# Performance work log

Measured on AMD Instinct MI355X. Metric: run time of the kernel, lower is better.

Reference implementation:

```python
import jax, jax.numpy as jnp
import numpy as np
from jax import lax

N_WAY, N_SUPPORT, N_QUERY = 16, 256, 512
D_IN, D_EMB = 4096, 1024
N_CLUSTERS, MAX_ITER = 5, 100


def setup_inputs() -> dict:
    key = jax.random.key(0)
    k1, k2, kw, kb = jax.random.split(key, 4)
    support = jax.random.normal(k1, (N_WAY, N_SUPPORT, D_IN), jnp.float32)
    query = jax.random.normal(k2, (N_WAY, N_QUERY, D_IN), jnp.float32)
    W = jax.random.normal(kw, (D_IN, D_EMB), jnp.float32) / np.float32(np.sqrt(D_IN))
    b = jax.random.normal(kb, (D_EMB,), jnp.float32) * 0.01
    return {"support": support, "query": query, "W": W, "b": b}


def _sqdist(x, c):
    # x [n,d], c [k,d] -> [n,k] squared euclidean distances
    return (jnp.sum(x * x, -1, keepdims=True)
            - 2.0 * (x @ c.T)
            + jnp.sum(c * c, -1))


def _kmeans(x, init):
    # x [n,d], init [k,d]; fixed-iteration Lloyd's kmeans (converged state is a
    # fixed point of the update, matching the torch early-break semantics).
    n = x.shape[0]
    ones = jnp.ones((n,), x.dtype)

    def step(c, _):
        assign = jnp.argmin(_sqdist(x, c), axis=1)              # [n]
        sums = jax.ops.segment_sum(x, assign, num_segments=N_CLUSTERS)
        cnt = jax.ops.segment_sum(ones, assign, num_segments=N_CLUSTERS)
        # empty cluster keeps its old centroid
        new_c = jnp.where(cnt[:, None] > 0,
                          sums / jnp.maximum(cnt, 1.0)[:, None], c)
        return new_c, None

    c, _ = lax.scan(step, init, None, length=MAX_ITER)
    return c


def _forward(support, query, W, b):
    # encoder: shared linear over flattened (n_way * n) rows
    s = (support.reshape(-1, D_IN) @ W + b).reshape(N_WAY, N_SUPPORT, D_EMB)
    q = (query.reshape(-1, D_IN) @ W + b).reshape(N_WAY, N_QUERY, D_EMB)

    # per-class kmeans init: random subset of that class's support embeddings
    keys = jax.random.split(jax.random.key(42), N_WAY)

    def init_fn(key, class_emb):
        idx = jax.random.permutation(key, N_SUPPORT)[:N_CLUSTERS]
        return class_emb[idx]

    inits = jax.vmap(init_fn)(keys, s)                 # [n_way, k, d]
    cluster_protos = jax.vmap(_kmeans)(s, inits)       # [n_way, k, d]
    class_protos = cluster_protos.mean(axis=1)         # [n_way, d]

    # cdist(query_emb [b,n,d], protos [c,d]) -> [b,n,c]
    d2 = (jnp.sum(q * q, -1)[..., None]
          - 2.0 * jnp.einsum('bnd,cd->bnc', q, class_protos)
          + jnp.sum(class_protos * class_protos, -1))
    distances = jnp.sqrt(jnp.maximum(d2, 0.0))
    return -distances                                  # logits [n_way, n_query, n_classes]


def reference(support, query, W, b):
    return _forward(support, query, W, b)
```

## Files before the change

kernel.cpp:

```cpp
#include <hip/hip_runtime.h>
#include <cstdint>
#include <cstddef>


typedef __attribute__((ext_vector_type(4))) float f32x4;
typedef __attribute__((ext_vector_type(8))) short s16x8;
typedef __attribute__((ext_vector_type(4))) short s16x4;
typedef __attribute__((ext_vector_type(8))) __bf16 bf16x8;

__device__ __forceinline__ unsigned short f2bf(float f) {
  unsigned u = __float_as_uint(f);
  return (unsigned short)((u + 0x7FFFu + ((u >> 16) & 1u)) >> 16);
}
__device__ __forceinline__ float bf2f(unsigned short h) {
  return __uint_as_float(((unsigned)h) << 16);
}

typedef const __attribute__((address_space(1))) void GV;
typedef __attribute__((address_space(3))) void LV;
__device__ __forceinline__ void gload_lds16(const void* g, void* l) {
  __builtin_amdgcn_global_load_lds((GV*)g, (LV*)l, 16, 0, 0);
}
__device__ __forceinline__ f32x4 mfma16(bf16x8 a, bf16x8 b, f32x4 c) {
  return __builtin_amdgcn_mfma_f32_16x16x32_bf16(a, b, c, 0, 0, 0);
}
__device__ __forceinline__ float wave_sum(float v) {
#pragma unroll
  for (int st = 1; st < 64; st <<= 1) v += __shfl_xor(v, st);
  return v;
}

__device__ __forceinline__ void tf2x32(unsigned k0, unsigned k1, unsigned x0,
                                       unsigned x1, unsigned& y0, unsigned& y1) {
  unsigned ks0 = k0, ks1 = k1, ks2 = k0 ^ k1 ^ 0x1BD11BDAu;
  x0 += ks0; x1 += ks1;
  const int rA[4] = {13, 15, 26, 6};
  const int rB[4] = {17, 29, 16, 24};
#define ROTL(v, d) (((v) << (d)) | ((v) >> (32 - (d))))
#define RG(R)                                     \
  _Pragma("unroll") for (int i = 0; i < 4; i++) { \
    x0 += x1; x1 = ROTL(x1, R[i]); x1 ^= x0;      \
  }
  RG(rA); x0 += ks1; x1 += ks2 + 1u;
  RG(rB); x0 += ks2; x1 += ks0 + 2u;
  RG(rA); x0 += ks0; x1 += ks1 + 3u;
  RG(rB); x0 += ks1; x1 += ks2 + 4u;
  RG(rA); x0 += ks2; x1 += ks0 + 5u;
#undef RG
#undef ROTL
  y0 = x0; y1 = x1;
}

__global__ __launch_bounds__(256) void prep_sw_k(
    const float* __restrict__ W, const float* __restrict__ sup,
    short* __restrict__ WhiT, short* __restrict__ WloT,
    short* __restrict__ Shi, short* __restrict__ Slo) {
  __shared__ float tile[64][65];
  int t = threadIdx.x;
  if (blockIdx.x < 1024) {
    int bk = blockIdx.x & 63, bn = blockIdx.x >> 6;
#pragma unroll
    for (int i = 0; i < 4; i++) {
      int row = i * 16 + (t >> 4);
      int col = (t & 15) * 4;
      f32x4 v =
          *(const f32x4*)(W + (size_t)(bk * 64 + row) * 1024 + bn * 64 + col);
      tile[row][col + 0] = v[0]; tile[row][col + 1] = v[1];
      tile[row][col + 2] = v[2]; tile[row][col + 3] = v[3];
    }
    __syncthreads();
#pragma unroll
    for (int i = 0; i < 4; i++) {
      int nrow = i * 16 + (t >> 4);
      int kcol = (t & 15) * 4;
      s16x4 hv, lv;
#pragma unroll
      for (int e = 0; e < 4; e++) {
        float v = tile[kcol + e][nrow];
        unsigned short h = f2bf(v);
        hv[e] = (short)h;
        lv[e] = (short)f2bf(v - bf2f(h));
      }
      size_t off = (size_t)(bn * 64 + nrow) * 4096 + bk * 64 + kcol;
      *(s16x4*)(WhiT + off) = hv;
      *(s16x4*)(WloT + off) = lv;
    }
  } else {
    const size_t sup_n8 = (size_t)4096 * 4096 / 8;
    size_t stride = (size_t)(gridDim.x - 1024) * 256;
    for (size_t gid = (size_t)(blockIdx.x - 1024) * 256 + t; gid < sup_n8;
         gid += stride) {
      const float* src = sup + gid * 8;
      f32x4 v0 = *(const f32x4*)src, v1 = *(const f32x4*)(src + 4);
      s16x8 h, l;
#pragma unroll
      for (int e = 0; e < 4; e++) {
        unsigned short hh = f2bf(v0[e]);
        h[e] = (short)hh; l[e] = (short)f2bf(v0[e] - bf2f(hh));
      }
#pragma unroll
      for (int e = 0; e < 4; e++) {
        unsigned short hh = f2bf(v1[e]);
        h[4 + e] = (short)hh; l[4 + e] = (short)f2bf(v1[e] - bf2f(hh));
      }
      *(s16x8*)(Shi + gid * 8) = h;
      *(s16x8*)(Slo + gid * 8) = l;
    }
  }
}

__global__ __launch_bounds__(256) void gemm_supq_k(
    const short* __restrict__ Shi, const short* __restrict__ Slo,
    const short* __restrict__ WhiT, const short* __restrict__ WloT,
    const float* __restrict__ bias, float* __restrict__ emb,
    const float* __restrict__ qry, short* __restrict__ Qhi) {
  __shared__ short lds[24576];
  const int t = threadIdx.x;
  if (blockIdx.x < 512) {
    short* Ah = lds;
    short* Al = lds + 4096;
    short* Bh = lds + 8192;
    short* Bl = lds + 16384;
    const int bid = blockIdx.x;
    const int bm = bid & 63, bn = bid >> 6;
    const int lane = t & 63, w = t >> 6;
    const int wr = w >> 1, wc = w & 1;
    const int fr = lane & 15, kg = lane >> 4;
    const int ls = lane >> 3, lc = lane & 7;
    const short* Ag = Shi + (size_t)bm * 64 * 4096;
    const short* Alg = Slo + (size_t)bm * 64 * 4096;
    f32x4 acc[2][4] = {};

    for (int kt = 0; kt < 64; ++kt) {
      const int k0 = kt * 64;
      __syncthreads();
      const int cch = (lc ^ ls) * 8;
#pragma unroll
      for (int j = 0; j < 2; j++) {
        int rowl = w * 16 + j * 8 + ls;
        size_t aoff = (size_t)rowl * 4096 + k0 + cch;
        int ldst = (w * 16 + j * 8) * 64;
        gload_lds16(Ag + aoff, Ah + ldst);
        gload_lds16(Alg + aoff, Al + ldst);
      }
#pragma unroll
      for (int j = 0; j < 4; j++) {
        int rowl = w * 32 + j * 8 + ls;
        size_t boff = (size_t)(bn * 128 + rowl) * 4096 + k0 + cch;
        int ldst = (w * 32 + j * 8) * 64;
        gload_lds16(WhiT + boff, Bh + ldst);
        gload_lds16(WloT + boff, Bl + ldst);
      }
      __syncthreads();
#pragma unroll
      for (int ks = 0; ks < 2; ++ks) {
        const int cx = ((ks * 4 + kg) ^ (fr & 7)) * 8;
        bf16x8 ahf[2], alf[2], bhf[4], blf[4];
#pragma unroll
        for (int mi = 0; mi < 2; mi++) {
          int arow = wr * 32 + mi * 16 + fr;
          ahf[mi] =
              __builtin_bit_cast(bf16x8, *(const s16x8*)(Ah + arow * 64 + cx));
          alf[mi] =
              __builtin_bit_cast(bf16x8, *(const s16x8*)(Al + arow * 64 + cx));
        }
#pragma unroll
        for (int ni = 0; ni < 4; ni++) {
          int brow = wc * 64 + ni * 16 + fr;
          bhf[ni] =
              __builtin_bit_cast(bf16x8, *(const s16x8*)(Bh + brow * 64 + cx));
          blf[ni] =
              __builtin_bit_cast(bf16x8, *(const s16x8*)(Bl + brow * 64 + cx));
        }
#pragma unroll
        for (int mi = 0; mi < 2; mi++)
#pragma unroll
          for (int ni = 0; ni < 4; ni++) {
            acc[mi][ni] = mfma16(ahf[mi], bhf[ni], acc[mi][ni]);
            acc[mi][ni] = mfma16(ahf[mi], blf[ni], acc[mi][ni]);
            acc[mi][ni] = mfma16(alf[mi], bhf[ni], acc[mi][ni]);
          }
      }
    }
#pragma unroll
    for (int ni = 0; ni < 4; ni++) {
      int gc = bn * 128 + wc * 64 + ni * 16 + fr;
      float bv = bias[gc];
#pragma unroll
      for (int mi = 0; mi < 2; mi++) {
        int gr = bm * 64 + wr * 32 + mi * 16 + kg * 4;
#pragma unroll
        for (int r = 0; r < 4; r++)
          emb[(size_t)(gr + r) * 1024 + gc] = acc[mi][ni][r] + bv;
      }
    }
  } else {
    const size_t qry_n8 = (size_t)8192 * 4096 / 8;
    size_t stride = (size_t)(gridDim.x - 512) * 256;
    for (size_t gid = (size_t)(blockIdx.x - 512) * 256 + t; gid < qry_n8;
         gid += stride) {
      const float* src = qry + gid * 8;
      f32x4 v0 = *(const f32x4*)src, v1 = *(const f32x4*)(src + 4);
      s16x8 h;
#pragma unroll
      for (int e = 0; e < 4; e++) h[e] = (short)f2bf(v0[e]);
#pragma unroll
      for (int e = 0; e < 4; e++) h[4 + e] = (short)f2bf(v1[e]);
      *(s16x8*)(Qhi + gid * 8) = h;
    }
  }
}

__global__ __launch_bounds__(256) void gemm_qry_diag_k(
    const short* __restrict__ Qhi, const short* __restrict__ WhiT,
    const float* __restrict__ bias, float* __restrict__ emb,
    float* __restrict__ G) {
  __shared__ short lds[16384];
  const int t = threadIdx.x;
  if (blockIdx.x < 512) {
    short* Ah = lds;
    short* Bh = lds + 8192;
    const int bid = blockIdx.x;
    const int bm = bid & 63, bn = bid >> 6;
    const int lane = t & 63, w = t >> 6;
    const int wr = w >> 1, wc = w & 1;
    const int fr = lane & 15, kg = lane >> 4;
    const int ls = lane >> 3, lc = lane & 7;
    const short* Ag = Qhi + (size_t)bm * 128 * 4096;
    f32x4 acc[4][4] = {};

    for (int kt = 0; kt < 64; ++kt) {
      const int k0 = kt * 64;
      __syncthreads();
      const int cch = (lc ^ ls) * 8;
#pragma unroll
      for (int j = 0; j < 4; j++) {
        int rowl = w * 32 + j * 8 + ls;
        size_t aoff = (size_t)rowl * 4096 + k0 + cch;
        size_t boff = (size_t)(bn * 128 + rowl) * 4096 + k0 + cch;
        int ldst = (w * 32 + j * 8) * 64;
        gload_lds16(Ag + aoff, Ah + ldst);
        gload_lds16(WhiT + boff, Bh + ldst);
      }
      __syncthreads();
#pragma unroll
      for (int ks = 0; ks < 2; ++ks) {
        const int cx = ((ks * 4 + kg) ^ (fr & 7)) * 8;
        bf16x8 ahf[4], bhf[4];
#pragma unroll
        for (int mi = 0; mi < 4; mi++) {
          int arow = wr * 64 + mi * 16 + fr;
          ahf[mi] =
              __builtin_bit_cast(bf16x8, *(const s16x8*)(Ah + arow * 64 + cx));
        }
#pragma unroll
        for (int ni = 0; ni < 4; ni++) {
          int brow = wc * 64 + ni * 16 + fr;
          bhf[ni] =
              __builtin_bit_cast(bf16x8, *(const s16x8*)(Bh + brow * 64 + cx));
        }
#pragma unroll
        for (int mi = 0; mi < 4; mi++)
#pragma unroll
          for (int ni = 0; ni < 4; ni++)
            acc[mi][ni] = mfma16(ahf[mi], bhf[ni], acc[mi][ni]);
      }
    }
#pragma unroll
    for (int ni = 0; ni < 4; ni++) {
      int gc = bn * 128 + wc * 64 + ni * 16 + fr;
      float bv = bias[gc];
#pragma unroll
      for (int mi = 0; mi < 4; mi++) {
        int gr = 4096 + bm * 128 + wr * 64 + mi * 16 + kg * 4;
#pragma unroll
        for (int r = 0; r < 4; r++)
          emb[(size_t)(gr + r) * 1024 + gc] = acc[mi][ni][r] + bv;
      }
    }
  } else {
    int r = (blockIdx.x - 512) * 4 + (t >> 6);
    int lane = t & 63;
    const float* x = emb + (size_t)r * 1024;
    double acc = 0.0;
#pragma unroll
    for (int ch = 0; ch < 16; ch++) {
      float v = x[ch * 64 + lane];
      acc = fma((double)v, (double)v, acc);
    }
#pragma unroll
    for (int st = 1; st < 64; st <<= 1) acc += __shfl_xor(acc, st);
    if (lane == 0) {
      int c = r >> 8, i = r & 255;
      G[(size_t)c * 65536 + (size_t)i * 256 + i] = (float)acc;
    }
  }
}

__global__ __launch_bounds__(256) void gram_km_k(const float* __restrict__ emb,
                                                 float* __restrict__ G) {
  int c = blockIdx.x >> 4, tl = blockIdx.x & 15, ti = tl >> 2, tj = tl & 3;
  __shared__ float AsT[32][68];
  __shared__ float BsT[32][68];
  int t = threadIdx.x, ty = t >> 4, tx = t & 15;
  const float* base = emb + (size_t)c * 256 * 1024;
  float acc[4][4] = {};
  for (int k0 = 0; k0 < 1024; k0 += 32) {
    __syncthreads();
    {
      int r = t >> 2, seg = t & 3;
      const float* pa = base + (size_t)(ti * 64 + r) * 1024 + k0 + seg * 8;
      f32x4 va0 = *(const f32x4*)pa, va1 = *(const f32x4*)(pa + 4);
#pragma unroll
      for (int e = 0; e < 4; e++) AsT[seg * 8 + e][r] = va0[e];
#pragma unroll
      for (int e = 0; e < 4; e++) AsT[seg * 8 + 4 + e][r] = va1[e];
      const float* pb = base + (size_t)(tj * 64 + r) * 1024 + k0 + seg * 8;
      f32x4 vb0 = *(const f32x4*)pb, vb1 = *(const f32x4*)(pb + 4);
#pragma unroll
      for (int e = 0; e < 4; e++) BsT[seg * 8 + e][r] = vb0[e];
#pragma unroll
      for (int e = 0; e < 4; e++) BsT[seg * 8 + 4 + e][r] = vb1[e];
    }
    __syncthreads();
#pragma unroll 4
    for (int kk = 0; kk < 32; kk++) {
      f32x4 av = *(const f32x4*)(&AsT[kk][ty * 4]);
      f32x4 bv = *(const f32x4*)(&BsT[kk][tx * 4]);
#pragma unroll
      for (int jdx = 0; jdx < 4; jdx++) {
        acc[0][jdx] = fmaf(av[0], bv[jdx], acc[0][jdx]);
        acc[1][jdx] = fmaf(av[1], bv[jdx], acc[1][jdx]);
        acc[2][jdx] = fmaf(av[2], bv[jdx], acc[2][jdx]);
        acc[3][jdx] = fmaf(av[3], bv[jdx], acc[3][jdx]);
      }
    }
  }
#pragma unroll
  for (int i = 0; i < 4; i++) {
    int gr = ti * 64 + ty * 4 + i;
#pragma unroll
    for (int j = 0; j < 4; j++) {
      int gcl = tj * 64 + tx * 4 + j;
      if (gr != gcl)
        G[(size_t)c * 65536 + (size_t)gr * 256 + gcl] = acc[i][j];
    }
  }
}

__global__ __launch_bounds__(256) void gemm_all_k(
    const float* __restrict__ sup, const float* __restrict__ qry,
    const short* __restrict__ WhiT, const short* __restrict__ WloT,
    const float* __restrict__ bias, float* __restrict__ emb) {
  __shared__ short lds[4 * 128 * 64];
  short* Ah = lds;
  short* Al = lds + 8192;
  short* Bh = lds + 16384;
  short* Bl = lds + 24576;
  const int bid = blockIdx.x;
  const int bm = bid % 96, bn = bid / 96;
  const bool is_sup = bm < 32;
  const int t = threadIdx.x, lane = t & 63, w = t >> 6;
  const int wr = w >> 1, wc = w & 1;
  const int fr = lane & 15, kg = lane >> 4;
  const float* Abase = is_sup ? (sup + (size_t)bm * 128 * 4096)
                              : (qry + (size_t)(bm - 32) * 128 * 4096);
  f32x4 acc[4][4] = {};
  const int ls = lane >> 3, lc = lane & 7;

  for (int kt = 0; kt < 64; ++kt) {
    const int k0 = kt * 64;
    __syncthreads();
#pragma unroll
    for (int i = 0; i < 4; i++) {
      int row = i * 32 + w * 8 + ls;
      const float* src = Abase + (size_t)row * 4096 + k0 + lc * 8;
      f32x4 v0 = *(const f32x4*)src;
      f32x4 v1 = *(const f32x4*)(src + 4);
      s16x8 hs;
#pragma unroll
      for (int e = 0; e < 4; e++) hs[e] = (short)f2bf(v0[e]);
#pragma unroll
      for (int e = 0; e < 4; e++) hs[4 + e] = (short)f2bf(v1[e]);
      int chunk = lc ^ (row & 7);
      *(s16x8*)(Ah + row * 64 + chunk * 8) = hs;
      if (is_sup) {
        s16x8 lsv;
#pragma unroll
        for (int e = 0; e < 4; e++)
          lsv[e] = (short)f2bf(v0[e] - bf2f((unsigned short)hs[e]));
#pragma unroll
        for (int e = 0; e < 4; e++)
          lsv[4 + e] = (short)f2bf(v1[e] - bf2f((unsigned short)hs[4 + e]));
        *(s16x8*)(Al + row * 64 + chunk * 8) = lsv;
      }
    }
#pragma unroll
    for (int j = 0; j < 4; j++) {
      int rowl = w * 32 + j * 8 + ls;
      int cch = (lc ^ (ls & 7)) * 8;
      size_t goff = (size_t)(bn * 128 + rowl) * 4096 + k0 + cch;
      gload_lds16(WhiT + goff, Bh + (w * 32 + j * 8) * 64);
      if (is_sup) gload_lds16(WloT + goff, Bl + (w * 32 + j * 8) * 64);
    }
    __syncthreads();
#pragma unroll
    for (int ks = 0; ks < 2; ++ks) {
      const int cx = ((ks * 4 + kg) ^ (fr & 7)) * 8;
      bf16x8 ahf[4], bhf[4];
#pragma unroll
      for (int mi = 0; mi < 4; mi++) {
        int arow = wr * 64 + mi * 16 + fr;
        ahf[mi] = __builtin_bit_cast(bf16x8, *(const s16x8*)(Ah + arow * 64 + cx));
      }
#pragma unroll
      for (int ni = 0; ni < 4; ni++) {
        int brow = wc * 64 + ni * 16 + fr;
        bhf[ni] = __builtin_bit_cast(bf16x8, *(const s16x8*)(Bh + brow * 64 + cx));
      }
      if (is_sup) {
        bf16x8 alf[4], blf[4];
#pragma unroll
        for (int mi = 0; mi < 4; mi++) {
          int arow = wr * 64 + mi * 16 + fr;
          alf[mi] =
              __builtin_bit_cast(bf16x8, *(const s16x8*)(Al + arow * 64 + cx));
        }
#pragma unroll
        for (int ni = 0; ni < 4; ni++) {
          int brow = wc * 64 + ni * 16 + fr;
          blf[ni] =
              __builtin_bit_cast(bf16x8, *(const s16x8*)(Bl + brow * 64 + cx));
        }
#pragma unroll
        for (int mi = 0; mi < 4; mi++)
#pragma unroll
          for (int ni = 0; ni < 4; ni++) {
            acc[mi][ni] = mfma16(ahf[mi], bhf[ni], acc[mi][ni]);
            acc[mi][ni] = mfma16(ahf[mi], blf[ni], acc[mi][ni]);
            acc[mi][ni] = mfma16(alf[mi], bhf[ni], acc[mi][ni]);
          }
      } else {
#pragma unroll
        for (int mi = 0; mi < 4; mi++)
#pragma unroll
          for (int ni = 0; ni < 4; ni++)
            acc[mi][ni] = mfma16(ahf[mi], bhf[ni], acc[mi][ni]);
      }
    }
  }
#pragma unroll
  for (int ni = 0; ni < 4; ni++) {
    int gc = bn * 128 + wc * 64 + ni * 16 + fr;
    float bv = bias[gc];
#pragma unroll
    for (int mi = 0; mi < 4; mi++) {
      int gr = bm * 128 + wr * 64 + mi * 16 + kg * 4;
#pragma unroll
      for (int r = 0; r < 4; r++)
        emb[(size_t)(gr + r) * 1024 + gc] = acc[mi][ni][r] + bv;
    }
  }
}

__global__ __launch_bounds__(256) void diag_k(const float* __restrict__ emb,
                                              float* __restrict__ G) {
  int r = blockIdx.x * 4 + (threadIdx.x >> 6);
  int lane = threadIdx.x & 63;
  const float* x = emb + (size_t)r * 1024;
  double acc = 0.0;
#pragma unroll
  for (int ch = 0; ch < 16; ch++) {
    float v = x[ch * 64 + lane];
    acc = fma((double)v, (double)v, acc);
  }
#pragma unroll
  for (int st = 1; st < 64; st <<= 1) acc += __shfl_xor(acc, st);
  if (lane == 0) {
    int c = r >> 8, i = r & 255;
    G[(size_t)c * 65536 + (size_t)i * 256 + i] = (float)acc;
  }
}

#define APPLY1(db, nb, gg, p)                        \
  if ((db) & 1u)  s[p][0] += ((nb) & 1u)  ? (gg) : -(gg); \
  if ((db) & 2u)  s[p][1] += ((nb) & 2u)  ? (gg) : -(gg); \
  if ((db) & 4u)  s[p][2] += ((nb) & 4u)  ? (gg) : -(gg); \
  if ((db) & 8u)  s[p][3] += ((nb) & 8u)  ? (gg) : -(gg); \
  if ((db) & 16u) s[p][4] += ((nb) & 16u) ? (gg) : -(gg);

__global__ __launch_bounds__(64) void kmeans3_k(const float* __restrict__ G,
                                                float* __restrict__ wts) {
  const int c = blockIdx.x;
  const int lane = threadIdx.x;
  unsigned o0, o1, s0k, s1k;
  tf2x32(0u, 42u, 0u, (unsigned)c, o0, o1);
  tf2x32(o0, o1, 0u, 1u, s0k, s1k);
  unsigned long long key[4];
#pragma unroll
  for (int q = 0; q < 4; q++) {
    unsigned y0, y1;
    tf2x32(s0k, s1k, 0u, (unsigned)(lane + 64 * q), y0, y1);
    key[q] = ((unsigned long long)(y0 ^ y1) << 32) | (unsigned)(lane + 64 * q);
  }
  int idx5[5];
#pragma unroll
  for (int r = 0; r < 5; r++) {
    unsigned long long mn = key[0];
#pragma unroll
    for (int q = 1; q < 4; q++) mn = key[q] < mn ? key[q] : mn;
#pragma unroll
    for (int st = 1; st < 64; st <<= 1) {
      unsigned long long o = __shfl_xor(mn, st);
      mn = o < mn ? o : mn;
    }
    int widx = (int)(unsigned)(mn & 0xffffffffu);
    idx5[r] = widx;
#pragma unroll
    for (int q = 0; q < 4; q++)
      if (widx == lane + 64 * q) key[q] = ~0ull;
  }
  unsigned m[4];
#pragma unroll
  for (int q = 0; q < 4; q++) {
    unsigned mm = 0;
#pragma unroll
    for (int k = 0; k < 5; k++)
      if (idx5[k] == lane + 64 * q) mm |= 1u << k;
    m[q] = mm;
  }
  const float* Gc = G + (size_t)c * 65536;
  float s[4][5];
#pragma unroll
  for (int k = 0; k < 5; k++) {
    const float* row = Gc + (size_t)idx5[k] * 256;
#pragma unroll
    for (int q = 0; q < 4; q++) s[q][k] = row[lane + 64 * q];
  }
  float Minv[5] = {1.0f, 1.0f, 1.0f, 1.0f, 1.0f};

  for (int it = 0; it < 100; ++it) {
    float Tu[5], C2[5];
#pragma unroll
    for (int k = 0; k < 5; k++) {
      float v = 0.0f;
#pragma unroll
      for (int q = 0; q < 4; q++)
        v += ((m[q] >> k) & 1u) ? s[q][k] : 0.0f;
#pragma unroll
      for (int st = 1; st < 64; st <<= 1) v += __shfl_xor(v, st);
      float iv = Minv[k];
      Tu[k] = v * iv * iv;
      C2[k] = -2.0f * iv;
    }
    int a[4];
#pragma unroll
    for (int q = 0; q < 4; q++) {
      float d0 = fmaf(C2[0], s[q][0], Tu[0]);
      float d1 = fmaf(C2[1], s[q][1], Tu[1]);
      float d2 = fmaf(C2[2], s[q][2], Tu[2]);
      float d3 = fmaf(C2[3], s[q][3], Tu[3]);
      float d4 = fmaf(C2[4], s[q][4], Tu[4]);
      int at = 0;
      float dmn = d0;
      if (d1 < dmn) { dmn = d1; at = 1; }
      if (d2 < dmn) { dmn = d2; at = 2; }
      if (d3 < dmn) { dmn = d3; at = 3; }
      if (d4 < dmn) { dmn = d4; at = 4; }
      a[q] = at;
    }
    int cnt[5];
#pragma unroll
    for (int k = 0; k < 5; k++) {
      int v = (a[0] == k) + (a[1] == k) + (a[2] == k) + (a[3] == k);
#pragma unroll
      for (int st = 1; st < 64; st <<= 1) v += __shfl_xor(v, st);
      cnt[k] = v;
    }
    unsigned nm[4], dm[4];
#pragma unroll
    for (int q = 0; q < 4; q++) {
      unsigned nv = 0;
#pragma unroll
      for (int k = 0; k < 5; k++) {
        int bit = (cnt[k] > 0) ? (a[q] == k ? 1 : 0) : (int)((m[q] >> k) & 1u);
        nv |= ((unsigned)bit) << k;
      }
      nm[q] = nv;
      dm[q] = nv ^ m[q];
    }
    unsigned long long bal[4];
#pragma unroll
    for (int q = 0; q < 4; q++) bal[q] = __ballot(dm[q] != 0);
    if ((bal[0] | bal[1] | bal[2] | bal[3]) == 0) break;
#pragma unroll
    for (int q = 0; q < 4; q++) m[q] = nm[q];
#pragma unroll
    for (int k = 0; k < 5; k++)
      if (cnt[k] > 0) Minv[k] = 1.0f / (float)cnt[k];
#pragma unroll
    for (int q = 0; q < 4; q++) {
      unsigned long long mask = bal[q];
      while (mask) {
#define GATHER(i)                                                      \
        int j##i = -1;                                                 \
        unsigned d##i = 0, e##i = 0;                                   \
        float g##i##0 = 0, g##i##1 = 0, g##i##2 = 0, g##i##3 = 0;      \
        if (mask) {                                                    \
          j##i = __builtin_ctzll(mask);                                \
          mask &= mask - 1;                                            \
          d##i = __shfl(dm[q], j##i);                                  \
          e##i = __shfl(nm[q], j##i);                                  \
          const float* row = Gc + (size_t)(q * 64 + j##i) * 256 + lane;\
          g##i##0 = row[0];  g##i##1 = row[64];                        \
          g##i##2 = row[128]; g##i##3 = row[192];                      \
        }
        GATHER(0) GATHER(1) GATHER(2) GATHER(3)
        GATHER(4) GATHER(5) GATHER(6) GATHER(7)
#undef GATHER
#define DOAPPLY(i)                        \
        if (j##i >= 0) {                  \
          APPLY1(d##i, e##i, g##i##0, 0)  \
          APPLY1(d##i, e##i, g##i##1, 1)  \
          APPLY1(d##i, e##i, g##i##2, 2)  \
          APPLY1(d##i, e##i, g##i##3, 3)  \
        }
        DOAPPLY(0) DOAPPLY(1) DOAPPLY(2) DOAPPLY(3)
        DOAPPLY(4) DOAPPLY(5) DOAPPLY(6) DOAPPLY(7)
#undef DOAPPLY
      }
    }
  }
#pragma unroll
  for (int q = 0; q < 4; q++) {
    float wv = 0.0f;
#pragma unroll
    for (int k = 0; k < 5; k++)
      if ((m[q] >> k) & 1u) wv += 0.2f * Minv[k];
    wts[c * 256 + lane + 64 * q] = wv;
  }
}

__global__ __launch_bounds__(256) void proto1_k(const float* __restrict__ emb,
                                                const float* __restrict__ wts,
                                                float* __restrict__ part) {
  int c = blockIdx.x & 15, seg = blockIdx.x >> 4, t = threadIdx.x;
  __shared__ float wl[16];
  if (t < 16) wl[t] = wts[c * 256 + seg * 16 + t];
  __syncthreads();
  f32x4 acc = {};
  const float* base = emb + (size_t)(c * 256 + seg * 16) * 1024 + t * 4;
#pragma unroll
  for (int j = 0; j < 16; j++) {
    f32x4 v = *(const f32x4*)(base + (size_t)j * 1024);
    float wj = wl[j];
#pragma unroll
    for (int e = 0; e < 4; e++) acc[e] = fmaf(wj, v[e], acc[e]);
  }
  *(f32x4*)(part + ((size_t)seg * 16 + c) * 1024 + t * 4) = acc;
}

__global__ __launch_bounds__(256) void proto2_k(const float* __restrict__ part,
                                                float* __restrict__ protos) {
  int c = blockIdx.x, t = threadIdx.x;
  f32x4 acc = {};
#pragma unroll
  for (int seg = 0; seg < 16; seg++) {
    f32x4 v = *(const f32x4*)(part + ((size_t)seg * 16 + c) * 1024 + t * 4);
#pragma unroll
    for (int e = 0; e < 4; e++) acc[e] += v[e];
  }
  *(f32x4*)(protos + (size_t)c * 1024 + t * 4) = acc;
}

__global__ __launch_bounds__(256) void proto_k(const float* __restrict__ emb,
                                               const float* __restrict__ wts,
                                               float* __restrict__ protos) {
  int c = blockIdx.x, t = threadIdx.x;
  __shared__ float wl[256];
  wl[t] = wts[c * 256 + t];
  __syncthreads();
  f32x4 acc = {};
  const float* base = emb + (size_t)c * 256 * 1024 + t * 4;
  for (int j = 0; j < 256; j++) {
    f32x4 v = *(const f32x4*)(base + (size_t)j * 1024);
    float wj = wl[j];
#pragma unroll
    for (int e = 0; e < 4; e++) acc[e] = fmaf(wj, v[e], acc[e]);
  }
  *(f32x4*)(protos + (size_t)c * 1024 + t * 4) = acc;
}

__global__ __launch_bounds__(256) void dist_k(const float* __restrict__ emb,
                                              const float* __restrict__ protos,
                                              float* __restrict__ out) {
  __shared__ float P[16 * 1024];
  int t = threadIdx.x, lane = t & 63, w = t >> 6;
#pragma unroll
  for (int i = 0; i < 16; i++) {
    int off = i * 1024 + t * 4;
    *(f32x4*)(P + off) = *(const f32x4*)(protos + off);
  }
  __syncthreads();
  float psq_keep = 0.0f;
  for (int p = 0; p < 16; p++) {
    float partial = 0.0f;
#pragma unroll
    for (int ch = 0; ch < 16; ch++) {
      float x = P[p * 1024 + ch * 64 + lane];
      partial = fmaf(x, x, partial);
    }
    partial = wave_sum(partial);
    if (lane == p) psq_keep = partial;
  }
  const float* qbase = emb + (size_t)4096 * 1024;
  int r0 = blockIdx.x * 16 + w * 4;
  for (int ri = 0; ri < 4; ri++) {
    int row = r0 + ri;
    const float* q = qbase + (size_t)row * 1024;
    float qv[16];
#pragma unroll
    for (int ch = 0; ch < 16; ch++) qv[ch] = q[ch * 64 + lane];
    float qsq = 0.0f;
#pragma unroll
    for (int ch = 0; ch < 16; ch++) qsq = fmaf(qv[ch], qv[ch], qsq);
    qsq = wave_sum(qsq);
    float dsel = 0.0f;
    for (int p = 0; p < 16; p++) {
      float dp = 0.0f;
#pragma unroll
      for (int ch = 0; ch < 16; ch++)
        dp = fmaf(qv[ch], P[p * 1024 + ch * 64 + lane], dp);
      dp = wave_sum(dp);
      if (lane == p) dsel = dp;
    }
    if (lane < 16) {
      float d2 = qsq - 2.0f * dsel + psq_keep;
      d2 = fmaxf(d2, 0.0f);
      out[(size_t)row * 16 + lane] = -sqrtf(d2);
    }
  }
}

extern "C" void kernel_launch(void* const* d_in, const int* in_sizes, int n_in,
                              void* d_out, int out_size, void* d_ws,
                              size_t ws_size, hipStream_t stream) {
  const float* sup = (const float*)d_in[0];
  const float* qry = (const float*)d_in[1];
  const float* W = (const float*)d_in[2];
  const float* b = (const float*)d_in[3];
  float* out = (float*)d_out;
  char* ws = (char*)d_ws;
  (void)in_sizes; (void)n_in; (void)out_size;

  const size_t NEED_FAST = 206651392ULL;
  if (ws_size >= NEED_FAST) {
    short* WhiT = (short*)(ws + 0);
    short* WloT = (short*)(ws + 8388608);
    short* Shi = (short*)(ws + 16777216);
    short* Slo = (short*)(ws + 50331648);
    short* Qhi = (short*)(ws + 83886080);
    float* emb = (float*)(ws + 150994944);
    float* G = (float*)(ws + 201326592);
    float* wts = (float*)(ws + 205520896);
    float* protos = (float*)(ws + 205537280);
    float* part = (float*)(ws + 205602816);

    prep_sw_k<<<2048, 256, 0, stream>>>(W, sup, WhiT, WloT, Shi, Slo);
    gemm_supq_k<<<768, 256, 0, stream>>>(Shi, Slo, WhiT, WloT, b, emb, qry,
                                         Qhi);
    gemm_qry_diag_k<<<1536, 256, 0, stream>>>(Qhi, WhiT, b, emb, G);
    gram_km_k<<<256, 256, 0, stream>>>(emb, G);
    kmeans3_k<<<16, 64, 0, stream>>>(G, wts);
    proto1_k<<<256, 256, 0, stream>>>(emb, wts, part);
    proto2_k<<<16, 256, 0, stream>>>(part, protos);
    dist_k<<<512, 256, 0, stream>>>(emb, protos, out);
  } else {
    short* WhiT = (short*)(ws + 0);
    short* WloT = (short*)(ws + 8388608);
    float* emb = (float*)(ws + 16777216);
    float* G = (float*)(ws + 67108864);
    float* wts = (float*)(ws + 71303168);
    float* protos = (float*)(ws + 71319552);

    prep_sw_k<<<1024, 256, 0, stream>>>(W, sup, WhiT, WloT, (short*)0,
                                        (short*)0);
    gemm_all_k<<<768, 256, 0, stream>>>(sup, qry, WhiT, WloT, b, emb);
    gram_km_k<<<256, 256, 0, stream>>>(emb, G);
    diag_k<<<1024, 256, 0, stream>>>(emb, G);
    kmeans3_k<<<16, 64, 0, stream>>>(G, wts);
    proto_k<<<16, 256, 0, stream>>>(emb, wts, protos);
    dist_k<<<512, 256, 0, stream>>>(emb, protos, out);
  }
}
```

Before: 446.3 us.

## Fuse query GEMM with distance computation and merge gram with diagonal kernel

The query-embedding GEMM is moved after the kmeans stage and now computes partial query-prototype dot products and squared norms straight from the accumulator tile, so the query embeddings are never written to global memory. A small reduction kernel combines the per-column-block partials with precomputed prototype norms to form the logits. The gram and diagonal kernels are merged into one launch. In exchange, the query GEMM no longer overlaps with the gram computation, the fused kernel uses more shared memory, and the distance is assembled from fp32 partial sums in a different order.

```diff
diff --git a/kernel.cpp b/kernel.cpp
--- a/kernel.cpp
+++ b/kernel.cpp
@@ -211,76 +211,59 @@
   }
 }
 
-__global__ __launch_bounds__(256) void gemm_qry_diag_k(
-    const short* __restrict__ Qhi, const short* __restrict__ WhiT,
-    const float* __restrict__ bias, float* __restrict__ emb,
-    float* __restrict__ G) {
-  __shared__ short lds[16384];
-  const int t = threadIdx.x;
-  if (blockIdx.x < 512) {
-    short* Ah = lds;
-    short* Bh = lds + 8192;
-    const int bid = blockIdx.x;
-    const int bm = bid & 63, bn = bid >> 6;
-    const int lane = t & 63, w = t >> 6;
-    const int wr = w >> 1, wc = w & 1;
-    const int fr = lane & 15, kg = lane >> 4;
-    const int ls = lane >> 3, lc = lane & 7;
-    const short* Ag = Qhi + (size_t)bm * 128 * 4096;
-    f32x4 acc[4][4] = {};
-
-    for (int kt = 0; kt < 64; ++kt) {
-      const int k0 = kt * 64;
+__global__ __launch_bounds__(256) void gramdiag2_k(const float* __restrict__ emb,
+                                                   float* __restrict__ G) {
+  if (blockIdx.x < 256) {
+    int c = blockIdx.x >> 4, tl = blockIdx.x & 15, ti = tl >> 2, tj = tl & 3;
+    __shared__ float AsT[32][68];
+    __shared__ float BsT[32][68];
+    int t = threadIdx.x, ty = t >> 4, tx = t & 15;
+    const float* base = emb + (size_t)c * 256 * 1024;
+    float acc[4][4] = {};
+    for (int k0 = 0; k0 < 1024; k0 += 32) {
       __syncthreads();
-      const int cch = (lc ^ ls) * 8;
+      {
+        int r = t >> 2, seg = t & 3;
+        const float* pa = base + (size_t)(ti * 64 + r) * 1024 + k0 + seg * 8;
+        f32x4 va0 = *(const f32x4*)pa, va1 = *(const f32x4*)(pa + 4);
+#pragma unroll
+        for (int e = 0; e < 4; e++) AsT[seg * 8 + e][r] = va0[e];
+#pragma unroll
+        for (int e = 0; e < 4; e++) AsT[seg * 8 + 4 + e][r] = va1[e];
+        const float* pb = base + (size_t)(tj * 64 + r) * 1024 + k0 + seg * 8;
+        f32x4 vb0 = *(const f32x4*)pb, vb1 = *(const f32x4*)(pb + 4);
+#pragma unroll
+        for (int e = 0; e < 4; e++) BsT[seg * 8 + e][r] = vb0[e];
+#pragma unroll
+        for (int e = 0; e < 4; e++) BsT[seg * 8 + 4 + e][r] = vb1[e];
+      }
+      __syncthreads();
+#pragma unroll 4
+      for (int kk = 0; kk < 32; kk++) {
+        f32x4 av = *(const f32x4*)(&AsT[kk][ty * 4]);
+        f32x4 bv = *(const f32x4*)(&BsT[kk][tx * 4]);
+#pragma unroll
+        for (int jdx = 0; jdx < 4; jdx++) {
+          acc[0][jdx] = fmaf(av[0], bv[jdx], acc[0][jdx]);
+          acc[1][jdx] = fmaf(av[1], bv[jdx], acc[1][jdx]);
+          acc[2][jdx] = fmaf(av[2], bv[jdx], acc[2][jdx]);
+          acc[3][jdx] = fmaf(av[3], bv[jdx], acc[3][jdx]);
+        }
+      }
+    }
+#pragma unroll
+    for (int i = 0; i < 4; i++) {
+      int gr = ti * 64 + ty * 4 + i;
 #pragma unroll
       for (int j = 0; j < 4; j++) {
-        int rowl = w * 32 + j * 8 + ls;
-        size_t aoff = (size_t)rowl * 4096 + k0 + cch;
-        size_t boff = (size_t)(bn * 128 + rowl) * 4096 + k0 + cch;
-        int ldst = (w * 32 + j * 8) * 64;
-        gload_lds16(Ag + aoff, Ah + ldst);
-        gload_lds16(WhiT + boff, Bh + ldst);
-      }
-      __syncthreads();
-#pragma unroll
-      for (int ks = 0; ks < 2; ++ks) {
-        const int cx = ((ks * 4 + kg) ^ (fr & 7)) * 8;
-        bf16x8 ahf[4], bhf[4];
-#pragma unroll
-        for (int mi = 0; mi < 4; mi++) {
-          int arow = wr * 64 + mi * 16 + fr;
-          ahf[mi] =
-              __builtin_bit_cast(bf16x8, *(const s16x8*)(Ah + arow * 64 + cx));
-        }
-#pragma unroll
-        for (int ni = 0; ni < 4; ni++) {
-          int brow = wc * 64 + ni * 16 + fr;
-          bhf[ni] =
-              __builtin_bit_cast(bf16x8, *(const s16x8*)(Bh + brow * 64 + cx));
-        }
-#pragma unroll
-        for (int mi = 0; mi < 4; mi++)
-#pragma unroll
-          for (int ni = 0; ni < 4; ni++)
-            acc[mi][ni] = mfma16(ahf[mi], bhf[ni], acc[mi][ni]);
-      }
-    }
-#pragma unroll
-    for (int ni = 0; ni < 4; ni++) {
-      int gc = bn * 128 + wc * 64 + ni * 16 + fr;
-      float bv = bias[gc];
-#pragma unroll
-      for (int mi = 0; mi < 4; mi++) {
-        int gr = 4096 + bm * 128 + wr * 64 + mi * 16 + kg * 4;
-#pragma unroll
-        for (int r = 0; r < 4; r++)
-          emb[(size_t)(gr + r) * 1024 + gc] = acc[mi][ni][r] + bv;
+        int gcl = tj * 64 + tx * 4 + j;
+        if (gr != gcl)
+          G[(size_t)c * 65536 + (size_t)gr * 256 + gcl] = acc[i][j];
       }
     }
   } else {
-    int r = (blockIdx.x - 512) * 4 + (t >> 6);
-    int lane = t & 63;
+    int r = (blockIdx.x - 256) * 4 + (threadIdx.x >> 6);
+    int lane = threadIdx.x & 63;
     const float* x = emb + (size_t)r * 1024;
     double acc = 0.0;
 #pragma unroll
@@ -293,57 +276,6 @@
     if (lane == 0) {
       int c = r >> 8, i = r & 255;
       G[(size_t)c * 65536 + (size_t)i * 256 + i] = (float)acc;
-    }
-  }
-}
-
-__global__ __launch_bounds__(256) void gram_km_k(const float* __restrict__ emb,
-                                                 float* __restrict__ G) {
-  int c = blockIdx.x >> 4, tl = blockIdx.x & 15, ti = tl >> 2, tj = tl & 3;
-  __shared__ float AsT[32][68];
-  __shared__ float BsT[32][68];
-  int t = threadIdx.x, ty = t >> 4, tx = t & 15;
-  const float* base = emb + (size_t)c * 256 * 1024;
-  float acc[4][4] = {};
-  for (int k0 = 0; k0 < 1024; k0 += 32) {
-    __syncthreads();
-    {
-      int r = t >> 2, seg = t & 3;
-      const float* pa = base + (size_t)(ti * 64 + r) * 1024 + k0 + seg * 8;
-      f32x4 va0 = *(const f32x4*)pa, va1 = *(const f32x4*)(pa + 4);
-#pragma unroll
-      for (int e = 0; e < 4; e++) AsT[seg * 8 + e][r] = va0[e];
-#pragma unroll
-      for (int e = 0; e < 4; e++) AsT[seg * 8 + 4 + e][r] = va1[e];
-      const float* pb = base + (size_t)(tj * 64 + r) * 1024 + k0 + seg * 8;
-      f32x4 vb0 = *(const f32x4*)pb, vb1 = *(const f32x4*)(pb + 4);
-#pragma unroll
-      for (int e = 0; e < 4; e++) BsT[seg * 8 + e][r] = vb0[e];
-#pragma unroll
-      for (int e = 0; e < 4; e++) BsT[seg * 8 + 4 + e][r] = vb1[e];
-    }
-    __syncthreads();
-#pragma unroll 4
-    for (int kk = 0; kk < 32; kk++) {
-      f32x4 av = *(const f32x4*)(&AsT[kk][ty * 4]);
-      f32x4 bv = *(const f32x4*)(&BsT[kk][tx * 4]);
-#pragma unroll
-      for (int jdx = 0; jdx < 4; jdx++) {
-        acc[0][jdx] = fmaf(av[0], bv[jdx], acc[0][jdx]);
-        acc[1][jdx] = fmaf(av[1], bv[jdx], acc[1][jdx]);
-        acc[2][jdx] = fmaf(av[2], bv[jdx], acc[2][jdx]);
-        acc[3][jdx] = fmaf(av[3], bv[jdx], acc[3][jdx]);
-      }
-    }
-  }
-#pragma unroll
-  for (int i = 0; i < 4; i++) {
-    int gr = ti * 64 + ty * 4 + i;
-#pragma unroll
-    for (int j = 0; j < 4; j++) {
-      int gcl = tj * 64 + tx * 4 + j;
-      if (gr != gcl)
-        G[(size_t)c * 65536 + (size_t)gr * 256 + gcl] = acc[i][j];
     }
   }
 }
@@ -460,25 +392,6 @@
       for (int r = 0; r < 4; r++)
         emb[(size_t)(gr + r) * 1024 + gc] = acc[mi][ni][r] + bv;
     }
-  }
-}
-
-__global__ __launch_bounds__(256) void diag_k(const float* __restrict__ emb,
-                                              float* __restrict__ G) {
-  int r = blockIdx.x * 4 + (threadIdx.x >> 6);
-  int lane = threadIdx.x & 63;
-  const float* x = emb + (size_t)r * 1024;
-  double acc = 0.0;
-#pragma unroll
-  for (int ch = 0; ch < 16; ch++) {
-    float v = x[ch * 64 + lane];
-    acc = fma((double)v, (double)v, acc);
-  }
-#pragma unroll
-  for (int st = 1; st < 64; st <<= 1) acc += __shfl_xor(acc, st);
-  if (lane == 0) {
-    int c = r >> 8, i = r & 255;
-    G[(size_t)c * 65536 + (size_t)i * 256 + i] = (float)acc;
   }
 }
 
@@ -660,9 +573,11 @@
   *(f32x4*)(part + ((size_t)seg * 16 + c) * 1024 + t * 4) = acc;
 }
 
-__global__ __launch_bounds__(256) void proto2_k(const float* __restrict__ part,
-                                                float* __restrict__ protos) {
-  int c = blockIdx.x, t = threadIdx.x;
+__global__ __launch_bounds__(256) void proto2p_k(const float* __restrict__ part,
+                                                 float* __restrict__ protos,
+                                                 float* __restrict__ psqb) {
+  __shared__ float Tp[4];
+  int c = blockIdx.x, t = threadIdx.x, lane = t & 63, w = t >> 6;
   f32x4 acc = {};
 #pragma unroll
   for (int seg = 0; seg < 16; seg++) {
@@ -671,6 +586,123 @@
     for (int e = 0; e < 4; e++) acc[e] += v[e];
   }
   *(f32x4*)(protos + (size_t)c * 1024 + t * 4) = acc;
+  float s = acc[0] * acc[0] + acc[1] * acc[1] + acc[2] * acc[2] +
+            acc[3] * acc[3];
+  s = wave_sum(s);
+  if (lane == 0) Tp[w] = s;
+  __syncthreads();
+  if (t == 0) psqb[c] = Tp[0] + Tp[1] + Tp[2] + Tp[3];
+}
+
+__global__ __launch_bounds__(256) void gemm_qry_dist_k(
+    const short* __restrict__ Qhi, const short* __restrict__ WhiT,
+    const float* __restrict__ bias, const float* __restrict__ protos,
+    float* __restrict__ part) {
+  __shared__ __align__(16) char smem[74496];
+  short* Ah = (short*)smem;
+  short* Bh = (short*)(smem + 16384);
+  float (*q_tile)[129] = (float(*)[129])smem;
+  float (*pl)[132] = (float(*)[132])(smem + 66048);
+  const int t = threadIdx.x;
+  const int bid = blockIdx.x;
+  const int bm = bid & 63, bn = bid >> 6;
+  const int lane = t & 63, w = t >> 6;
+  const int wr = w >> 1, wc = w & 1;
+  const int fr = lane & 15, kg = lane >> 4;
+  const int ls = lane >> 3, lc = lane & 7;
+  const short* Ag = Qhi + (size_t)bm * 128 * 4096;
+  f32x4 acc[4][4] = {};
+
+  for (int kt = 0; kt < 64; ++kt) {
+    const int k0 = kt * 64;
+    __syncthreads();
+    const int cch = (lc ^ ls) * 8;
+#pragma unroll
+    for (int j = 0; j < 4; j++) {
+      int rowl = w * 32 + j * 8 + ls;
+      size_t aoff = (size_t)rowl * 4096 + k0 + cch;
+      size_t boff = (size_t)(bn * 128 + rowl) * 4096 + k0 + cch;
+      int ldst = (w * 32 + j * 8) * 64;
+      gload_lds16(Ag + aoff, Ah + ldst);
+      gload_lds16(WhiT + boff, Bh + ldst);
+    }
+    __syncthreads();
+#pragma unroll
+    for (int ks = 0; ks < 2; ++ks) {
+      const int cx = ((ks * 4 + kg) ^ (fr & 7)) * 8;
+      bf16x8 ahf[4], bhf[4];
+#pragma unroll
+      for (int mi = 0; mi < 4; mi++) {
+        int arow = wr * 64 + mi * 16 + fr;
+        ahf[mi] = __builtin_bit_cast(bf16x8, *(const s16x8*)(Ah + arow * 64 + cx));
+      }
+#pragma unroll
+      for (int ni = 0; ni < 4; ni++) {
+        int brow = wc * 64 + ni * 16 + fr;
+        bhf[ni] = __builtin_bit_cast(bf16x8, *(const s16x8*)(Bh + brow * 64 + cx));
+      }
+#pragma unroll
+      for (int mi = 0; mi < 4; mi++)
+#pragma unroll
+        for (int ni = 0; ni < 4; ni++)
+          acc[mi][ni] = mfma16(ahf[mi], bhf[ni], acc[mi][ni]);
+    }
+  }
+  __syncthreads();
+#pragma unroll
+  for (int ni = 0; ni < 4; ni++) {
+    int cl = wc * 64 + ni * 16 + fr;
+    float bv = bias[bn * 128 + cl];
+#pragma unroll
+    for (int mi = 0; mi < 4; mi++) {
+      int rl = wr * 64 + mi * 16 + kg * 4;
+#pragma unroll
+      for (int r = 0; r < 4; r++) q_tile[rl + r][cl] = acc[mi][ni][r] + bv;
+    }
+  }
+  {
+    int p = t >> 4, cl0 = (t & 15) * 8;
+    const float* src = protos + (size_t)p * 1024 + bn * 128 + cl0;
+    f32x4 v0 = *(const f32x4*)src, v1 = *(const f32x4*)(src + 4);
+#pragma unroll
+    for (int e = 0; e < 4; e++) pl[p][cl0 + e] = v0[e];
+#pragma unroll
+    for (int e = 0; e < 4; e++) pl[p][cl0 + 4 + e] = v1[e];
+  }
+  __syncthreads();
+  const int row = t & 127, half = t >> 7;
+  float dot[16] = {};
+  float qs = 0.0f;
+#pragma unroll 4
+  for (int ci = 0; ci < 64; ci++) {
+    int c = half * 64 + ci;
+    float v = q_tile[row][c];
+    qs = fmaf(v, v, qs);
+#pragma unroll
+    for (int p = 0; p < 16; p++) dot[p] = fmaf(v, pl[p][c], dot[p]);
+  }
+  int grow = bm * 128 + row;
+  float* dst = part + ((size_t)(bn * 2 + half) * 8192 + grow) * 17;
+#pragma unroll
+  for (int p = 0; p < 16; p++) dst[p] = dot[p];
+  dst[16] = qs;
+}
+
+__global__ __launch_bounds__(256) void distred_k(const float* __restrict__ part,
+                                                 const float* __restrict__ psqb,
+                                                 float* __restrict__ out) {
+  int gid = blockIdx.x * 256 + threadIdx.x;
+  int row = gid >> 4, p = gid & 15;
+  float dot = 0.0f, qs = 0.0f;
+#pragma unroll
+  for (int s = 0; s < 16; s++) {
+    const float* src = part + ((size_t)s * 8192 + row) * 17;
+    dot += src[p];
+    qs += src[16];
+  }
+  float d2 = qs - 2.0f * dot + psqb[p];
+  d2 = fmaxf(d2, 0.0f);
+  out[(size_t)row * 16 + p] = -sqrtf(d2);
 }
 
 __global__ __launch_bounds__(256) void proto_k(const float* __restrict__ emb,
@@ -764,17 +796,19 @@
     float* G = (float*)(ws + 201326592);
     float* wts = (float*)(ws + 205520896);
     float* protos = (float*)(ws + 205537280);
-    float* part = (float*)(ws + 205602816);
+    float* part1 = (float*)(ws + 205602816);
+    float* dpart = (float*)(ws + 16777216);
+    float* psqb = (float*)(ws + 50331648);
 
     prep_sw_k<<<2048, 256, 0, stream>>>(W, sup, WhiT, WloT, Shi, Slo);
     gemm_supq_k<<<768, 256, 0, stream>>>(Shi, Slo, WhiT, WloT, b, emb, qry,
                                          Qhi);
-    gemm_qry_diag_k<<<1536, 256, 0, stream>>>(Qhi, WhiT, b, emb, G);
-    gram_km_k<<<256, 256, 0, stream>>>(emb, G);
+    gramdiag2_k<<<1280, 256, 0, stream>>>(emb, G);
     kmeans3_k<<<16, 64, 0, stream>>>(G, wts);
-    proto1_k<<<256, 256, 0, stream>>>(emb, wts, part);
-    proto2_k<<<16, 256, 0, stream>>>(part, protos);
-    dist_k<<<512, 256, 0, stream>>>(emb, protos, out);
+    proto1_k<<<256, 256, 0, stream>>>(emb, wts, part1);
+    proto2p_k<<<16, 256, 0, stream>>>(part1, protos, psqb);
+    gemm_qry_dist_k<<<512, 256, 0, stream>>>(Qhi, WhiT, b, protos, dpart);
+    distred_k<<<512, 256, 0, stream>>>(dpart, psqb, out);
   } else {
     short* WhiT = (short*)(ws + 0);
     short* WloT = (short*)(ws + 8388608);
@@ -786,8 +820,7 @@
     prep_sw_k<<<1024, 256, 0, stream>>>(W, sup, WhiT, WloT, (short*)0,
                                         (short*)0);
     gemm_all_k<<<768, 256, 0, stream>>>(sup, qry, WhiT, WloT, b, emb);
-    gram_km_k<<<256, 256, 0, stream>>>(emb, G);
-    diag_k<<<1024, 256, 0, stream>>>(emb, G);
+    gramdiag2_k<<<1280, 256, 0, stream>>>(emb, G);
     kmeans3_k<<<16, 64, 0, stream>>>(G, wts);
     proto_k<<<16, 256, 0, stream>>>(emb, wts, protos);
     dist_k<<<512, 256, 0, stream>>>(emb, protos, out);
```

After: 408.8 us. 1.09x faster.
